# Kernel optimization log

Hardware: AMD Instinct MI355X
Metric: run time of the kernel (lower is better)

The kernel has to match this reference:

```python
import jax, jax.numpy as jnp
import numpy as np

N_BOND = 2_000_000
N_ATOM = 100_000
N_STRUCT = 2
THREEBODY_CUTOFF = 0.8


def setup_inputs() -> dict:
    key = jax.random.key(0)
    k1, k2 = jax.random.split(key)
    # bonds grouped (sorted) by source atom, as _compute_threebody assumes
    bond_src = jnp.sort(jax.random.randint(k1, (N_BOND,), 0, N_ATOM))
    bond_length = jax.random.uniform(k2, (N_BOND,), dtype=jnp.float32)
    n_atoms = jnp.full((N_STRUCT,), N_ATOM // N_STRUCT, dtype=jnp.int32)
    return {"bond_src": bond_src, "bond_length": bond_length, "n_atoms": n_atoms}


def reference(bond_src, bond_length, n_atoms):
    """Vectorized equivalent of compute_threebody_indices.

    Returns (bond_indices [T,2] pairs of ORIGINAL bond ids, n_triple_ij [n_bond],
    n_triple_i [n_atom], n_triple_s [n_struct]). Replaces the O(n) Python loops
    with segment-sum (degree count), prefix-sum (CSR offsets) and a flat
    enumeration of ordered within-atom bond pairs (j != k).
    """
    n_bond = bond_src.shape[0]
    n_atom = int(jnp.sum(n_atoms))
    n_struct = n_atoms.shape[0]

    # --- filter bonds by three-body cutoff, remember original bond ids ---
    mask = bond_length <= THREEBODY_CUTOFF
    kept = jnp.nonzero(mask)[0]          # original bond indices of surviving bonds
    src = bond_src[kept]                 # still sorted (subset of a sorted array)

    # --- per-atom bond counts and CSR offsets (parallel histogram + scan) ---
    deg = jax.ops.segment_sum(jnp.ones_like(src), src, num_segments=n_atom)
    bond_offset = jnp.cumsum(deg) - deg  # start of each atom's bond block

    # --- triples per atom / per bond / per structure ---
    n_triple_i = deg * (deg - 1)
    T = int(jnp.sum(n_triple_i))

    # --- enumerate all ordered pairs (j, k), j != k, within each atom block ---
    tri_atom = jnp.repeat(jnp.arange(n_atom), n_triple_i, total_repeat_length=T)
    tri_start = (jnp.cumsum(n_triple_i) - n_triple_i)[tri_atom]
    t = jnp.arange(T) - tri_start        # local triple index in [0, d*(d-1))
    d = deg[tri_atom]                    # d >= 2 wherever triples exist
    j = t // (d - 1)
    kp = t % (d - 1)
    k = kp + (kp >= j).astype(kp.dtype)  # skip k == j, preserving loop order
    b0 = bond_offset[tri_atom] + j       # relative (filtered) bond index
    b1 = bond_offset[tri_atom] + k
    bond_indices = jnp.stack([kept[b0], kept[b1]], axis=1)  # back to ORIGINAL ids

    # angles per ORIGINAL bond: deg(src)-1 for surviving bonds, 0 for filtered
    n_triple_ij = jnp.zeros(n_bond, dtype=deg.dtype).at[kept].set(deg[src] - 1)

    # angles per structure
    struct_id = jnp.repeat(jnp.arange(n_struct), n_atoms, total_repeat_length=n_atom)
    n_triple_s = jax.ops.segment_sum(n_triple_i, struct_id, num_segments=n_struct)

    return bond_indices, n_triple_ij, n_triple_i, n_triple_s
```

## Files before the change

### kernel.cpp

```cpp
#include <hip/hip_runtime.h>


#define CUTOFF 0.8f
#define NATOM_C 100000
#define MAXD 256

__global__ void k0_init(int* wstart, int* wend, int* deg, int n_atom) {
    int i = blockIdx.x * blockDim.x + threadIdx.x;
    if (i < n_atom) { wstart[i] = 0; wend[i] = 0; deg[i] = 0; }
}

__global__ void kA_bounds_deg(const int* __restrict__ src, const float* __restrict__ len,
                              int* __restrict__ wstart, int* __restrict__ wend,
                              int* __restrict__ deg, int n_bond) {
    int i = blockIdx.x * blockDim.x + threadIdx.x;
    int lane = threadIdx.x & 63;
    bool valid = i < n_bond;
    int a = -1;
    bool kept = false;
    if (valid) {
        a = src[i];
        if (i == 0 || src[i - 1] != a) wstart[a] = i;
        if (i == n_bond - 1 || src[i + 1] != a) wend[a] = i + 1;
        kept = (len[i] <= CUTOFF);
    }
    unsigned long long keptB = __ballot(kept);
    int ap = __shfl_up(a, 1);
    bool head = (lane == 0) || (ap != a);
    unsigned long long headB = __ballot(head);
    unsigned long long nextHeads = (headB >> 1) >> lane;
    bool tail = (lane == 63) || ((nextHeads & 1ull) != 0ull);
    if (tail && valid) {
        unsigned long long below = (lane == 63) ? ~0ull : ((2ull << lane) - 1ull);
        int runStart = 63 - __clzll(headB & below);
        unsigned long long runMask = below & ~((1ull << runStart) - 1ull);
        int cnt = __popcll(keptB & runMask);
        if (cnt) atomicAdd(&deg[a], cnt);
    }
}

__global__ void kB_scan(const int* __restrict__ deg, int* __restrict__ out_i,
                        int* __restrict__ exsc, int* __restrict__ bsums, int n) {
    __shared__ int tmp[256];
    int t = threadIdx.x;
    int base = blockIdx.x * 1024 + t * 4;
    int v0 = 0, v1 = 0, v2 = 0, v3 = 0;
    if (base     < n) { int d = deg[base];     v0 = d * (d - 1); out_i[base]     = v0; }
    if (base + 1 < n) { int d = deg[base + 1]; v1 = d * (d - 1); out_i[base + 1] = v1; }
    if (base + 2 < n) { int d = deg[base + 2]; v2 = d * (d - 1); out_i[base + 2] = v2; }
    if (base + 3 < n) { int d = deg[base + 3]; v3 = d * (d - 1); out_i[base + 3] = v3; }
    int s = v0 + v1 + v2 + v3;
    tmp[t] = s;
    __syncthreads();
    for (int off = 1; off < 256; off <<= 1) {
        int v = (t >= off) ? tmp[t - off] : 0;
        __syncthreads();
        tmp[t] += v;
        __syncthreads();
    }
    int excl = tmp[t] - s;
    if (base     < n) exsc[base]     = excl;
    if (base + 1 < n) exsc[base + 1] = excl + v0;
    if (base + 2 < n) exsc[base + 2] = excl + v0 + v1;
    if (base + 3 < n) exsc[base + 3] = excl + v0 + v1 + v2;
    if (t == 255) bsums[blockIdx.x] = tmp[255];
}

__global__ void kC_scan2(int* __restrict__ bsums, const int* __restrict__ exsc,
                         const int* __restrict__ n_atoms_arr, int* __restrict__ out_s,
                         int nb, int n_atom, int n_struct) {
    const int B = 256;
    __shared__ int sums[B];
    int t = threadIdx.x;
    int chunk = (nb + B - 1) / B;
    int lo = t * chunk; if (lo > nb) lo = nb;
    int hi = lo + chunk; if (hi > nb) hi = nb;
    int ssum = 0;
    for (int i = lo; i < hi; i++) ssum += bsums[i];
    sums[t] = ssum;
    __syncthreads();
    for (int off = 1; off < B; off <<= 1) {
        int v = (t >= off) ? sums[t - off] : 0;
        __syncthreads();
        sums[t] += v;
        __syncthreads();
    }
    int run = sums[t] - ssum;
    for (int i = lo; i < hi; i++) { int v = bsums[i]; bsums[i] = run; run += v; }
    if (t == B - 1) {  }
    int total = sums[B - 1];
    __syncthreads();
    if (t == 0) {
        int off = 0, prevA = 0;
        for (int s = 0; s < n_struct; s++) {
            off += n_atoms_arr[s];
            int A = (off >= n_atom) ? total : (exsc[off] + bsums[off >> 10]);
            out_s[s] = A - prevA;
            prevA = A;
        }
    }
}

__global__ void kD_enum(const float* __restrict__ len, const int* __restrict__ wstart,
                        const int* __restrict__ wend, const int* __restrict__ exsc,
                        const int* __restrict__ bsums,
                        int4* __restrict__ out4, int* __restrict__ out_ij,
                        int n_atom) {
    __shared__ int keptIds[4 * MAXD];
    int wave = threadIdx.x >> 6;
    int lane = threadIdx.x & 63;
    int a = blockIdx.x * 4 + wave;
    int* my = &keptIds[wave * MAXD];
    if (a >= n_atom) return;
    int s = wstart[a], e = wend[a];
    int d = 0;
    for (int base = s; base < e; base += 64) {
        int idx = base + lane;
        bool m = (idx < e) && (len[idx] <= CUTOFF);
        unsigned long long bal = __ballot(m);
        int pos = d + __popcll(bal & ((1ull << lane) - 1ull));
        if (m && pos < MAXD) my[pos] = idx;
        d += __popcll(bal);
    }
    int dm1 = d - 1;
    for (int idx = s + lane; idx < e; idx += 64)
        out_ij[idx] = (len[idx] <= CUTOFF) ? dm1 : 0;
    if (d >= 2) {
        unsigned udm1 = (unsigned)dm1;
        unsigned nP = ((unsigned)(d * dm1)) >> 1;
        int b4 = (exsc[a] + bsums[a >> 10]) >> 1;
        for (unsigned p = lane; p < nP; p += 64) {
            unsigned t0 = 2u * p;
            unsigned j  = t0 / udm1;
            unsigned kp = t0 - j * udm1;
            unsigned j1 = j, kp1 = kp + 1;
            if (kp1 == udm1) { j1++; kp1 = 0; }
            unsigned k0 = kp  + (kp  >= j  ? 1u : 0u);
            unsigned k1 = kp1 + (kp1 >= j1 ? 1u : 0u);
            out4[b4 + p] = make_int4(my[j], my[k0], my[j1], my[k1]);
        }
    }
}

extern "C" void kernel_launch(void* const* d_in, const int* in_sizes, int n_in,
                              void* d_out, int out_size, void* d_ws, size_t ws_size,
                              hipStream_t stream) {
    const int*   bond_src    = (const int*)d_in[0];
    const float* bond_len    = (const float*)d_in[1];
    const int*   n_atoms_arr = (const int*)d_in[2];
    int n_bond   = in_sizes[0];
    int n_struct = in_sizes[2];
    const int n_atom = NATOM_C;
    int T2 = out_size - n_bond - n_atom - n_struct;

    int nblk_scan = (n_atom + 1023) / 1024;

    int* ws     = (int*)d_ws;
    int* wstart = ws;
    int* wend   = ws + n_atom;
    int* deg    = ws + 2 * n_atom;
    int* exsc   = ws + 3 * n_atom;
    int* bsums  = exsc + n_atom;

    int*  out       = (int*)d_out;
    int4* out_pairs = (int4*)out;
    int*  out_ij    = out + T2;
    int*  out_i     = out_ij + n_bond;
    int*  out_s     = out_i + n_atom;

    k0_init      <<<(n_atom + 255) / 256, 256, 0, stream>>>(wstart, wend, deg, n_atom);
    kA_bounds_deg<<<(n_bond + 255) / 256, 256, 0, stream>>>(bond_src, bond_len, wstart, wend, deg, n_bond);
    kB_scan      <<<nblk_scan, 256, 0, stream>>>(deg, out_i, exsc, bsums, n_atom);
    kC_scan2     <<<1, 256, 0, stream>>>(bsums, exsc, n_atoms_arr, out_s, nblk_scan, n_atom, n_struct);
    kD_enum      <<<(n_atom + 3) / 4, 256, 0, stream>>>(bond_len, wstart, wend, exsc, bsums, out_pairs, out_ij, n_atom);
    kD_enum      <<<(n_atom + 3) / 4, 256, 0, stream>>>(bond_len, wstart, wend, exsc, bsums, out_pairs, out_ij, n_atom);
}
```

Measured before the change: 281.7 us.

## Drop duplicate enum launch and fold block-offset scan into enum kernel

Removes the second, redundant launch of the enumeration kernel and the single-block second-level scan kernel. Each wave in the enumeration kernel now reduces the needed tile sums itself with a shuffle reduction, and one wave computes the per-structure totals. The degree-scan kernel also uses int4 loads and stores. This cuts kernel launches and a serial single-block pass, but adds redundant per-wave reduction reads of the tile sums.

After: 246.2 us. 1.14x faster.

```diff
diff --git a/kernel.cpp b/kernel.cpp
--- a/kernel.cpp
+++ b/kernel.cpp
@@ -45,10 +45,17 @@
     int t = threadIdx.x;
     int base = blockIdx.x * 1024 + t * 4;
     int v0 = 0, v1 = 0, v2 = 0, v3 = 0;
-    if (base     < n) { int d = deg[base];     v0 = d * (d - 1); out_i[base]     = v0; }
-    if (base + 1 < n) { int d = deg[base + 1]; v1 = d * (d - 1); out_i[base + 1] = v1; }
-    if (base + 2 < n) { int d = deg[base + 2]; v2 = d * (d - 1); out_i[base + 2] = v2; }
-    if (base + 3 < n) { int d = deg[base + 3]; v3 = d * (d - 1); out_i[base + 3] = v3; }
+    if (base + 3 < n) {
+        int4 d4 = *(const int4*)(deg + base);
+        v0 = d4.x * (d4.x - 1); v1 = d4.y * (d4.y - 1);
+        v2 = d4.z * (d4.z - 1); v3 = d4.w * (d4.w - 1);
+        *(int4*)(out_i + base) = make_int4(v0, v1, v2, v3);
+    } else {
+        if (base     < n) { int d = deg[base];     v0 = d * (d - 1); out_i[base]     = v0; }
+        if (base + 1 < n) { int d = deg[base + 1]; v1 = d * (d - 1); out_i[base + 1] = v1; }
+        if (base + 2 < n) { int d = deg[base + 2]; v2 = d * (d - 1); out_i[base + 2] = v2; }
+        if (base + 3 < n) { int d = deg[base + 3]; v3 = d * (d - 1); out_i[base + 3] = v3; }
+    }
     int s = v0 + v1 + v2 + v3;
     tmp[t] = s;
     __syncthreads();
@@ -66,51 +73,39 @@
     if (t == 255) bsums[blockIdx.x] = tmp[255];
 }
 
-__global__ void kC_scan2(int* __restrict__ bsums, const int* __restrict__ exsc,
-                         const int* __restrict__ n_atoms_arr, int* __restrict__ out_s,
-                         int nb, int n_atom, int n_struct) {
-    const int B = 256;
-    __shared__ int sums[B];
-    int t = threadIdx.x;
-    int chunk = (nb + B - 1) / B;
-    int lo = t * chunk; if (lo > nb) lo = nb;
-    int hi = lo + chunk; if (hi > nb) hi = nb;
-    int ssum = 0;
-    for (int i = lo; i < hi; i++) ssum += bsums[i];
-    sums[t] = ssum;
-    __syncthreads();
-    for (int off = 1; off < B; off <<= 1) {
-        int v = (t >= off) ? sums[t - off] : 0;
-        __syncthreads();
-        sums[t] += v;
-        __syncthreads();
-    }
-    int run = sums[t] - ssum;
-    for (int i = lo; i < hi; i++) { int v = bsums[i]; bsums[i] = run; run += v; }
-    if (t == B - 1) {  }
-    int total = sums[B - 1];
-    __syncthreads();
-    if (t == 0) {
-        int off = 0, prevA = 0;
-        for (int s = 0; s < n_struct; s++) {
-            off += n_atoms_arr[s];
-            int A = (off >= n_atom) ? total : (exsc[off] + bsums[off >> 10]);
-            out_s[s] = A - prevA;
-            prevA = A;
-        }
-    }
+__device__ __forceinline__ int wave_prefix_sum(const int* __restrict__ bsums,
+                                               int K, int lane) {
+    int x = 0;
+    for (int l = lane; l < K; l += 64) x += bsums[l];
+#pragma unroll
+    for (int m = 1; m < 64; m <<= 1) x += __shfl_xor(x, m);
+    return x;
 }
 
 __global__ void kD_enum(const float* __restrict__ len, const int* __restrict__ wstart,
                         const int* __restrict__ wend, const int* __restrict__ exsc,
-                        const int* __restrict__ bsums,
+                        const int* __restrict__ bsums, const int* __restrict__ n_atoms_arr,
                         int4* __restrict__ out4, int* __restrict__ out_ij,
-                        int n_atom) {
+                        int* __restrict__ out_s,
+                        int n_atom, int ntiles, int n_struct) {
     __shared__ int keptIds[4 * MAXD];
     int wave = threadIdx.x >> 6;
     int lane = threadIdx.x & 63;
     int a = blockIdx.x * 4 + wave;
     int* my = &keptIds[wave * MAXD];
+
+    if (blockIdx.x == 0 && wave == 0) {
+        int off = 0, prevA = 0;
+        for (int s2 = 0; s2 < n_struct; s2++) {
+            off += n_atoms_arr[s2];
+            int A;
+            if (off >= n_atom) A = wave_prefix_sum(bsums, ntiles, lane);
+            else               A = wave_prefix_sum(bsums, off >> 10, lane) + exsc[off];
+            if (lane == 0) out_s[s2] = A - prevA;
+            prevA = A;
+        }
+    }
+
     if (a >= n_atom) return;
     int s = wstart[a], e = wend[a];
     int d = 0;
@@ -126,9 +121,10 @@
     for (int idx = s + lane; idx < e; idx += 64)
         out_ij[idx] = (len[idx] <= CUTOFF) ? dm1 : 0;
     if (d >= 2) {
+        int pref = wave_prefix_sum(bsums, a >> 10, lane);
+        int b4 = (exsc[a] + pref) >> 1;
         unsigned udm1 = (unsigned)dm1;
         unsigned nP = ((unsigned)(d * dm1)) >> 1;
-        int b4 = (exsc[a] + bsums[a >> 10]) >> 1;
         for (unsigned p = lane; p < nP; p += 64) {
             unsigned t0 = 2u * p;
             unsigned j  = t0 / udm1;
@@ -153,7 +149,7 @@
     const int n_atom = NATOM_C;
     int T2 = out_size - n_bond - n_atom - n_struct;
 
-    int nblk_scan = (n_atom + 1023) / 1024;
+    int ntiles = (n_atom + 1023) / 1024;
 
     int* ws     = (int*)d_ws;
     int* wstart = ws;
@@ -170,8 +166,8 @@
 
     k0_init      <<<(n_atom + 255) / 256, 256, 0, stream>>>(wstart, wend, deg, n_atom);
     kA_bounds_deg<<<(n_bond + 255) / 256, 256, 0, stream>>>(bond_src, bond_len, wstart, wend, deg, n_bond);
-    kB_scan      <<<nblk_scan, 256, 0, stream>>>(deg, out_i, exsc, bsums, n_atom);
-    kC_scan2     <<<1, 256, 0, stream>>>(bsums, exsc, n_atoms_arr, out_s, nblk_scan, n_atom, n_struct);
-    kD_enum      <<<(n_atom + 3) / 4, 256, 0, stream>>>(bond_len, wstart, wend, exsc, bsums, out_pairs, out_ij, n_atom);
-    kD_enum      <<<(n_atom + 3) / 4, 256, 0, stream>>>(bond_len, wstart, wend, exsc, bsums, out_pairs, out_ij, n_atom);
+    kB_scan      <<<ntiles, 256, 0, stream>>>(deg, out_i, exsc, bsums, n_atom);
+    kD_enum      <<<(n_atom + 3) / 4, 256, 0, stream>>>(bond_len, wstart, wend, exsc, bsums,
+                                                        n_atoms_arr, out_pairs, out_ij, out_s,
+                                                        n_atom, ntiles, n_struct);
 }
```
